# Optimization experiments

Hardware: AMD Instinct MI355X
Metric: run time of the kernel (lower is better)

The kernel has to match this reference:

```python
import jax, jax.numpy as jnp
import numpy as np

DIM = 256
B = 8
H = 56
W = 56
K = 2
EPS = 1e-5  # torch BatchNorm2d default eps


def _conv1x1(x, w, b):
    # x: [B,C,H,W], w: [O,C], b: [O]
    return jnp.einsum('oc,bchw->bohw', w, x) + b[None, :, None, None]


def _bn(x, g, be, m, v):
    # inference-mode BatchNorm2d with running stats
    s = g / jnp.sqrt(v + EPS)
    return x * s[None, :, None, None] + (be - m * s)[None, :, None, None]


def _grapher(x, w1, b1, g1, be1, m1, v1, wg, bg, gg, beg, mg, vg, w2, b2, g2, be2, m2, v2):
    # fc1: 1x1 conv + BN
    h = _bn(_conv1x1(x, w1, b1), g1, be1, m1, v1)
    Hh, Ww = h.shape[2], h.shape[3]
    # MRConv4d: running max over circular-shift differences
    # torch.cat([x[:,:,-i:,:], x[:,:,:-i,:]], dim=2) == jnp.roll(x, i, axis=2)
    xj = jnp.zeros_like(h)

    def body_h(c, i):
        return jnp.maximum(c, h - jnp.roll(h, i, axis=2)), None

    xj, _ = jax.lax.scan(body_h, xj, jnp.arange(K, Hh, K))

    def body_w(c, i):
        return jnp.maximum(c, h - jnp.roll(h, i, axis=3)), None

    xj, _ = jax.lax.scan(body_w, xj, jnp.arange(K, Ww, K))

    cat = jnp.concatenate([h, xj], axis=1)  # [B, 2*dim, H, W]
    # MRConv4d.nn: Conv2d(2*dim, 2*dim, 1) -> BN(2*dim) -> GELU (exact erf)
    g = jax.nn.gelu(_bn(_conv1x1(cat, wg, bg), gg, beg, mg, vg), approximate=False)
    # fc2: Conv2d(2*dim, dim, 1) + BN(dim), then residual
    return _bn(_conv1x1(g, w2, b2), g2, be2, m2, v2) + x


def setup_inputs() -> dict:
    key = jax.random.key(0)
    ks = jax.random.split(key, 12)
    d, d2 = DIM, 2 * DIM

    def w(k, o, c):
        return jax.random.normal(k, (o, c), jnp.float32) * np.float32(1.0 / np.sqrt(c))

    return {
        'x': jax.random.normal(ks[0], (B, d, H, W), jnp.float32),
        'w1': w(ks[1], d, d), 'b1': jnp.zeros((d,), jnp.float32),
        'g1': jnp.ones((d,), jnp.float32), 'be1': jnp.zeros((d,), jnp.float32),
        'm1': jax.random.normal(ks[2], (d,), jnp.float32) * 0.1,
        'v1': jax.random.uniform(ks[3], (d,), jnp.float32, 0.5, 1.5),
        'wg': w(ks[4], d2, d2), 'bg': jnp.zeros((d2,), jnp.float32),
        'gg': jnp.ones((d2,), jnp.float32), 'beg': jnp.zeros((d2,), jnp.float32),
        'mg': jax.random.normal(ks[5], (d2,), jnp.float32) * 0.1,
        'vg': jax.random.uniform(ks[6], (d2,), jnp.float32, 0.5, 1.5),
        'w2': w(ks[7], d, d2), 'b2': jnp.zeros((d,), jnp.float32),
        'g2': jnp.ones((d,), jnp.float32), 'be2': jnp.zeros((d,), jnp.float32),
        'm2': jax.random.normal(ks[8], (d,), jnp.float32) * 0.1,
        'v2': jax.random.uniform(ks[9], (d,), jnp.float32, 0.5, 1.5),
    }


def reference(x, w1, b1, g1, be1, m1, v1, wg, bg, gg, beg, mg, vg, w2, b2, g2, be2, m2, v2):
    return _grapher(x, w1, b1, g1, be1, m1, v1, wg, bg, gg, beg, mg, vg, w2, b2, g2, be2, m2, v2)
```

## Files before the change

### kernel.cpp

```cpp
#include <hip/hip_runtime.h>
#include <math.h>

#define SPB 3136
#define NB 8
#define MTOT (NB*SPB)
#define EPS 1e-5f

typedef unsigned short u16;
typedef __attribute__((ext_vector_type(8))) short short8;
typedef __attribute__((ext_vector_type(4))) float float4v;

__device__ __forceinline__ float b2f(u16 v){ unsigned u=((unsigned)v)<<16; float f; __builtin_memcpy(&f,&u,4); return f; }
__device__ __forceinline__ u16 f2b(float f){ unsigned u; __builtin_memcpy(&u,&f,4); u += 0x7fffu + ((u>>16)&1u); return (u16)(u>>16); }
__device__ __forceinline__ float gelu_f(float z){ return 0.5f*z*(1.0f+erff(z*0.70710678118654752f)); }

__device__ __forceinline__ void gll16(const u16* g, u16* l){
  __builtin_amdgcn_global_load_lds((const __attribute__((address_space(1))) void*)g,
                                   (__attribute__((address_space(3))) void*)l, 16, 0, 0);
}

__global__ void prep_consts_k(const float* b1,const float* g1,const float* be1,const float* m1,const float* v1,
                              const float* bg,const float* gg,const float* beg,const float* mg,const float* vg,
                              const float* b2,const float* g2,const float* be2,const float* m2,const float* v2,
                              float* cst){
  int i = threadIdx.x;
  if (i < 256) {
    float s = g1[i]*rsqrtf(v1[i]+EPS);
    cst[i] = s; cst[256+i] = b1[i]*s + be1[i] - m1[i]*s;
    float s2 = g2[i]*rsqrtf(v2[i]+EPS);
    cst[1536+i] = s2; cst[1792+i] = b2[i]*s2 + be2[i] - m2[i]*s2;
  }
  float s = gg[i]*rsqrtf(vg[i]+EPS);
  cst[512+i] = s; cst[1024+i] = bg[i]*s + beg[i] - mg[i]*s;
}

__global__ void conv_w_k(const float* __restrict__ w1,const float* __restrict__ wg,const float* __restrict__ w2,
                         u16* __restrict__ w1b,u16* __restrict__ wgb,u16* __restrict__ w2b){
  int i = blockIdx.x*256 + threadIdx.x;
  if (i < 65536)  w1b[i] = f2b(w1[i]);
  if (i < 262144) wgb[i] = f2b(wg[i]);
  if (i < 131072) w2b[i] = f2b(w2[i]);
}

__global__ void transpose_x_k(const float* __restrict__ x, u16* __restrict__ xt){
  __shared__ float t[32][33];
  int b = blockIdx.z, ct = blockIdx.y, st = blockIdx.x;
  int ts = threadIdx.x, tc = threadIdx.y;
  #pragma unroll
  for (int i=0;i<4;i++){
    int c = tc + i*8;
    t[c][ts] = x[((size_t)(b*256 + ct*32 + c))*SPB + st*32 + ts];
  }
  __syncthreads();
  #pragma unroll
  for (int i=0;i<4;i++){
    int r = tc + i*8;
    xt[((size_t)(b*SPB + st*32 + r))*256 + ct*32 + ts] = f2b(t[ts][r]);
  }
}

__global__ void rowmin_k(const u16* __restrict__ cat, float* __restrict__ rmin){
  int b = blockIdx.x/56, y = blockIdx.x%56, c = threadIdx.x;
  float mE=3.4e38f, mO=3.4e38f;
  const u16* base = cat + ((size_t)(b*SPB + y*56))*512 + c;
  for (int x=0;x<56;x+=2){
    mE = fminf(mE, b2f(base[(size_t)x*512]));
    mO = fminf(mO, b2f(base[(size_t)(x+1)*512]));
  }
  rmin[((size_t)(b*2+0)*56 + y)*256 + c]=mE;
  rmin[((size_t)(b*2+1)*56 + y)*256 + c]=mO;
}
__global__ void colmin_k(const u16* __restrict__ cat, float* __restrict__ cmin){
  int b = blockIdx.x/56, x = blockIdx.x%56, c = threadIdx.x;
  float mE=3.4e38f, mO=3.4e38f;
  const u16* base = cat + ((size_t)(b*SPB + x))*512 + c;
  for (int y=0;y<56;y+=2){
    mE = fminf(mE, b2f(base[(size_t)(y*56)*512]));
    mO = fminf(mO, b2f(base[(size_t)((y+1)*56)*512]));
  }
  cmin[((size_t)(b*2+0)*56 + x)*256 + c]=mE;
  cmin[((size_t)(b*2+1)*56 + x)*256 + c]=mO;
}
__global__ void xj_k(u16* __restrict__ cat, const float* __restrict__ rmin, const float* __restrict__ cmin){
  int b = blockIdx.y, s = blockIdx.x, c = threadIdx.x;
  int y = s/56, x = s%56;
  size_t idx = ((size_t)(b*SPB + s))*512;
  float h = b2f(cat[idx + c]);
  float m = fminf(cmin[((size_t)(b*2+(y&1))*56 + x)*256 + c],
                  rmin[((size_t)(b*2+(x&1))*56 + y)*256 + c]);
  cat[idx + 256 + c] = f2b(fmaxf(0.0f, h - m));
}

template<int KTOT, int EPI>
__global__ __launch_bounds__(256) void gemm_k(
    const u16* __restrict__ Ain, const u16* __restrict__ Wt,
    const float* __restrict__ scale, const float* __restrict__ bias,
    void* __restrict__ outp, const float* __restrict__ resid)
{
  __shared__ __align__(16) u16 smem[16896];
  u16* As = smem;
  u16* Bs = smem + 4096;
  const int tid = threadIdx.x;
  const int m0 = blockIdx.x * 128;
  const int o0 = blockIdx.y * 128;
  const int lane = tid & 63, wid = tid >> 6;
  const int quad = lane >> 4, l16 = lane & 15;
  const int wm = wid & 1, wn = wid >> 1;

  float4v acc[4][4];
  #pragma unroll
  for (int i=0;i<4;i++)
    #pragma unroll
    for (int j=0;j<4;j++) acc[i][j] = (float4v){0.f,0.f,0.f,0.f};

  const int row = tid >> 2, q8 = (tid & 3) * 8;
  const u16* ga0 = Ain + ((size_t)(m0 + row))*KTOT + q8;
  const u16* ga1 = ga0 + (size_t)64*KTOT;
  const u16* gb0 = Wt  + ((size_t)(o0 + row))*KTOT + q8;
  const u16* gb1 = gb0 + (size_t)64*KTOT;
  u16* la0 = As + tid*8;
  u16* la1 = As + 2048 + tid*8;
  u16* lb0 = Bs + tid*8;
  u16* lb1 = Bs + 2048 + tid*8;

  for (int kt = 0; kt < KTOT; kt += 32) {
    gll16(ga0 + kt, la0);
    gll16(ga1 + kt, la1);
    gll16(gb0 + kt, lb0);
    gll16(gb1 + kt, lb1);
    __syncthreads();
    short8 af[4], bfr[4];
    #pragma unroll
    for (int im=0;im<4;im++) af[im]  = *(const short8*)&As[(wm*64+im*16+l16)*32 + quad*8];
    #pragma unroll
    for (int in=0;in<4;in++) bfr[in] = *(const short8*)&Bs[(wn*64+in*16+l16)*32 + quad*8];
    #pragma unroll
    for (int im=0;im<4;im++)
      #pragma unroll
      for (int in=0;in<4;in++)
        acc[im][in] = __builtin_amdgcn_mfma_f32_16x16x32_bf16(af[im], bfr[in], acc[im][in], 0, 0, 0);
    __syncthreads();
  }

  if (EPI == 1 || EPI == 2) {
    u16* tile = smem;
    #pragma unroll
    for (int im=0;im<4;im++)
      #pragma unroll
      for (int in=0;in<4;in++){
        int ol = wn*64 + in*16 + l16;
        float sc = scale[o0+ol], bi = bias[o0+ol];
        #pragma unroll
        for (int r=0;r<4;r++){
          float v = acc[im][in][r]*sc + bi;
          if (EPI==2) v = gelu_f(v);
          tile[(wm*64+im*16+quad*4+r)*128 + ol] = f2b(v);
        }
      }
    __syncthreads();
    u16* op = (u16*)outp;
    #pragma unroll
    for (int p=0;p<8;p++){
      int chunk = p*256 + tid;
      int rr = chunk >> 4, off = (chunk & 15)*8;
      *(uint4*)&op[((size_t)(m0 + rr))*512 + o0 + off] = *(const uint4*)&tile[rr*128 + off];
    }
  } else {
    float* ftile = (float*)smem;
    float* op = (float*)outp;
    #pragma unroll
    for (int h=0; h<2; h++){
      if (wn == h){
        #pragma unroll
        for (int im=0;im<4;im++)
          #pragma unroll
          for (int in=0;in<4;in++){
            int c64 = in*16 + l16;
            int og = o0 + h*64 + c64;
            float sc = scale[og], bi = bias[og];
            float4v v;
            #pragma unroll
            for (int r=0;r<4;r++) v[r] = acc[im][in][r]*sc + bi;
            *(float4v*)&ftile[c64*132 + wm*64 + im*16 + quad*4] = v;
          }
      }
      __syncthreads();
      #pragma unroll
      for (int p=0;p<8;p++){
        int chunk = p*256 + tid;
        int rr = chunk >> 5, off = (chunk & 31)*4;
        int m = m0 + off;
        int b = m / SPB, s = m - b*SPB;
        size_t g = ((size_t)(b*256 + o0 + h*64 + rr))*SPB + s;
        float4v v = *(const float4v*)&ftile[rr*132 + off];
        v.x += resid[g]; v.y += resid[g+1]; v.z += resid[g+2]; v.w += resid[g+3];
        *(float4v*)&op[g] = v;
      }
      __syncthreads();
    }
  }
}

extern "C" void kernel_launch(void* const* d_in, const int* in_sizes, int n_in,
                              void* d_out, int out_size, void* d_ws, size_t ws_size,
                              hipStream_t stream)
{
  const float* x  = (const float*)d_in[0];
  const float* w1 = (const float*)d_in[1];
  const float* b1 = (const float*)d_in[2];
  const float* g1 = (const float*)d_in[3];
  const float* be1= (const float*)d_in[4];
  const float* m1 = (const float*)d_in[5];
  const float* v1 = (const float*)d_in[6];
  const float* wg = (const float*)d_in[7];
  const float* bg = (const float*)d_in[8];
  const float* gg = (const float*)d_in[9];
  const float* beg= (const float*)d_in[10];
  const float* mg = (const float*)d_in[11];
  const float* vg = (const float*)d_in[12];
  const float* w2 = (const float*)d_in[13];
  const float* b2 = (const float*)d_in[14];
  const float* g2 = (const float*)d_in[15];
  const float* be2= (const float*)d_in[16];
  const float* m2 = (const float*)d_in[17];
  const float* v2 = (const float*)d_in[18];

  char* ws = (char*)d_ws;
  size_t off = 0;
  auto alloc = [&](size_t bytes){ void* p = ws + off; off += (bytes + 255) & ~(size_t)255; return p; };
  u16* xt    = (u16*)alloc((size_t)MTOT*256*2);
  u16* catt  = (u16*)alloc((size_t)MTOT*512*2);
  u16* gt    = (u16*)alloc((size_t)MTOT*512*2);
  u16* w1b   = (u16*)alloc((size_t)65536*2);
  u16* wgb   = (u16*)alloc((size_t)262144*2);
  u16* w2b   = (u16*)alloc((size_t)131072*2);
  float* cst = (float*)alloc((size_t)2048*4);
  float* rmin= (float*)alloc((size_t)NB*2*56*256*4);
  float* cmin= (float*)alloc((size_t)NB*2*56*256*4);

  hipLaunchKernelGGL(prep_consts_k, dim3(1), dim3(512), 0, stream,
                     b1,g1,be1,m1,v1, bg,gg,beg,mg,vg, b2,g2,be2,m2,v2, cst);
  hipLaunchKernelGGL(conv_w_k, dim3(1024), dim3(256), 0, stream, w1,wg,w2, w1b,wgb,w2b);
  hipLaunchKernelGGL(transpose_x_k, dim3(98,8,8), dim3(32,8), 0, stream, x, xt);
  hipLaunchKernelGGL((gemm_k<256,1>), dim3(196,2), dim3(256), 0, stream,
                     xt, w1b, cst+0, cst+256, (void*)catt, (const float*)nullptr);
  hipLaunchKernelGGL(rowmin_k, dim3(NB*56), dim3(256), 0, stream, catt, rmin);
  hipLaunchKernelGGL(colmin_k, dim3(NB*56), dim3(256), 0, stream, catt, cmin);
  hipLaunchKernelGGL(xj_k, dim3(SPB, NB), dim3(256), 0, stream, catt, rmin, cmin);
  hipLaunchKernelGGL((gemm_k<512,2>), dim3(196,4), dim3(256), 0, stream,
                     catt, wgb, cst+512, cst+1024, (void*)gt, (const float*)nullptr);
  hipLaunchKernelGGL((gemm_k<512,3>), dim3(196,2), dim3(256), 0, stream,
                     gt, w2b, cst+1536, cst+1792, d_out, x);
}
```

Before: 206.1 us.

## Double-buffer GEMM K-loop LDS staging and use tanh-form GELU

The GEMM main loop now double-buffers LDS tiles, issuing the global-to-LDS loads for the next K-step before running the MFMAs on the current one, with one barrier per iteration. This overlaps load latency with compute. Separately, the exact erf GELU is replaced with the tanh approximation written as a sigmoid using fast exp and divide. That is cheaper per element but deviates from the exact-erf reference, so it risks exceeding the accuracy tolerance.

After: 195.3 us. 1.06x faster.

```diff
diff --git a/kernel.cpp b/kernel.cpp
--- a/kernel.cpp
+++ b/kernel.cpp
@@ -12,7 +12,10 @@
 
 __device__ __forceinline__ float b2f(u16 v){ unsigned u=((unsigned)v)<<16; float f; __builtin_memcpy(&f,&u,4); return f; }
 __device__ __forceinline__ u16 f2b(float f){ unsigned u; __builtin_memcpy(&u,&f,4); u += 0x7fffu + ((u>>16)&1u); return (u16)(u>>16); }
-__device__ __forceinline__ float gelu_f(float z){ return 0.5f*z*(1.0f+erff(z*0.70710678118654752f)); }
+__device__ __forceinline__ float gelu_f(float z){
+  float t = 1.5957691216f * z * (1.0f + 0.044715f*z*z);
+  return __fdividef(z, 1.0f + __expf(-t));
+}
 
 __device__ __forceinline__ void gll16(const u16* g, u16* l){
   __builtin_amdgcn_global_load_lds((const __attribute__((address_space(1))) void*)g,
@@ -98,8 +101,6 @@
     void* __restrict__ outp, const float* __restrict__ resid)
 {
   __shared__ __align__(16) u16 smem[16896];
-  u16* As = smem;
-  u16* Bs = smem + 4096;
   const int tid = threadIdx.x;
   const int m0 = blockIdx.x * 128;
   const int o0 = blockIdx.y * 128;
@@ -118,29 +119,41 @@
   const u16* ga1 = ga0 + (size_t)64*KTOT;
   const u16* gb0 = Wt  + ((size_t)(o0 + row))*KTOT + q8;
   const u16* gb1 = gb0 + (size_t)64*KTOT;
-  u16* la0 = As + tid*8;
-  u16* la1 = As + 2048 + tid*8;
-  u16* lb0 = Bs + tid*8;
-  u16* lb1 = Bs + 2048 + tid*8;
-
-  for (int kt = 0; kt < KTOT; kt += 32) {
-    gll16(ga0 + kt, la0);
-    gll16(ga1 + kt, la1);
-    gll16(gb0 + kt, lb0);
-    gll16(gb1 + kt, lb1);
-    __syncthreads();
+  u16* l8 = smem + tid*8;
+
+  auto STAGE = [&](int kt, int buf){
+    u16* b_ = l8 + buf*8192;
+    gll16(ga0 + kt, b_);
+    gll16(ga1 + kt, b_ + 2048);
+    gll16(gb0 + kt, b_ + 4096);
+    gll16(gb1 + kt, b_ + 6144);
+  };
+  auto COMPUTE = [&](int buf){
+    const u16* A_ = smem + buf*8192;
+    const u16* B_ = A_ + 4096;
     short8 af[4], bfr[4];
     #pragma unroll
-    for (int im=0;im<4;im++) af[im]  = *(const short8*)&As[(wm*64+im*16+l16)*32 + quad*8];
-    #pragma unroll
-    for (int in=0;in<4;in++) bfr[in] = *(const short8*)&Bs[(wn*64+in*16+l16)*32 + quad*8];
+    for (int im=0;im<4;im++) af[im]  = *(const short8*)&A_[(wm*64+im*16+l16)*32 + quad*8];
+    #pragma unroll
+    for (int in=0;in<4;in++) bfr[in] = *(const short8*)&B_[(wn*64+in*16+l16)*32 + quad*8];
     #pragma unroll
     for (int im=0;im<4;im++)
       #pragma unroll
       for (int in=0;in<4;in++)
         acc[im][in] = __builtin_amdgcn_mfma_f32_16x16x32_bf16(af[im], bfr[in], acc[im][in], 0, 0, 0);
+  };
+
+  constexpr int NIT = KTOT / 32;
+  STAGE(0, 0);
+  __syncthreads();
+  #pragma unroll
+  for (int t = 1; t < NIT; ++t) {
+    STAGE(t*32, t & 1);
+    COMPUTE((t-1) & 1);
     __syncthreads();
   }
+  COMPUTE((NIT-1) & 1);
+  __syncthreads();
 
   if (EPI == 1 || EPI == 2) {
     u16* tile = smem;
```
